# Optimization experiments

Hardware: AMD Instinct MI355X
Metric: run time of the kernel (lower is better)

Reference implementation:

```python
import jax, jax.numpy as jnp
import numpy as np

_EPS = 1e-6
B, N, W, R, NW = 64, 1024, 64, 4, 1


def _cosine_weights(memory, keys, strengths):
    # memory: [B,N,W], keys: [B,H,W], strengths: [B,H] -> [B,H,N]
    dot = jnp.einsum('bhw,bnw->bhn', keys, memory)
    mem_norm = jnp.sqrt(jnp.sum(memory * memory, axis=-1) + _EPS)  # [B,N]
    key_norm = jnp.sqrt(jnp.sum(keys * keys, axis=-1) + _EPS)      # [B,H]
    sim = dot / (key_norm[:, :, None] * mem_norm[:, None, :] + _EPS)
    sharp = sim * jax.nn.softplus(strengths)[:, :, None]
    return jax.nn.softmax(sharp, axis=-1)


def _allocation(usage):
    # usage: [B,N] -> allocation weights [B,N] (DNC sort-based free-list)
    usage = _EPS + (1.0 - _EPS) * usage
    nonusage = 1.0 - usage
    sorted_nonusage, indices = jax.lax.top_k(nonusage, N)
    sorted_usage = 1.0 - sorted_nonusage
    prod_excl = jnp.concatenate(
        [jnp.ones_like(sorted_usage[:, :1]), jnp.cumprod(sorted_usage[:, :-1], axis=-1)], axis=-1)
    sorted_alloc = sorted_nonusage * prod_excl
    inv_perm = jnp.argsort(indices, axis=-1)  # batch_invert_permutation
    return jnp.take_along_axis(sorted_alloc, inv_perm, axis=-1)  # batch_gather


def _forward(memory, prev_read_weights, prev_write_weights, prev_usage, prev_link,
             prev_precedence, read_keys, read_strengths, write_keys, write_strengths,
             write_vectors, erase_vectors, free_gate, alloc_gate, write_gate, read_mode):
    # ---- usage update (Freeness.call); prev write weights are stop-gradient'd ----
    ww = jax.lax.stop_gradient(prev_write_weights)
    agg_write = 1.0 - jnp.prod(1.0 - ww, axis=1)                       # [B,N]
    usage = prev_usage + (1.0 - prev_usage) * agg_write
    phi = jnp.prod(1.0 - free_gate[:, :, None] * prev_read_weights, axis=1)
    usage = usage * phi
    # ---- write weights: content + allocation ----
    write_content = _cosine_weights(memory, write_keys, write_strengths)  # [B,NW,N]
    wg = alloc_gate * write_gate                                          # [B,NW]
    allocs = []
    u = usage
    for i in range(NW):  # fixed small head loop
        a = _allocation(u)
        allocs.append(a)
        u = u + (1.0 - u) * wg[:, i:i + 1] * a
    alloc_w = jnp.stack(allocs, axis=1)                                   # [B,NW,N]
    ag = alloc_gate[:, :, None]
    write_weights = write_gate[:, :, None] * (ag * alloc_w + (1.0 - ag) * write_content)
    # ---- erase + write memory ----
    reset = jnp.prod(1.0 - write_weights[:, :, :, None] * erase_vectors[:, :, None, :], axis=1)
    memory_new = memory * reset + jnp.einsum('bwn,bwk->bnk', write_weights, write_vectors)
    # ---- temporal link matrix update ----
    wi = write_weights[:, :, :, None]   # [B,NW,N,1]
    wj = write_weights[:, :, None, :]   # [B,NW,1,N]
    new_link = (1.0 - wi - wj) * prev_link + wi * prev_precedence[:, :, None, :]
    link = new_link * (1.0 - jnp.eye(N, dtype=memory.dtype))[None, None]  # zero diagonal
    # (precedence update, part of new state; not needed for read_words output)
    precedence = (1.0 - jnp.sum(write_weights, axis=-1, keepdims=True)) * prev_precedence + write_weights
    del precedence
    # ---- read weights: content + directional (forward/backward along link) ----
    read_content = _cosine_weights(memory_new, read_keys, read_strengths)   # [B,R,N]
    fwd_w = jnp.einsum('brm,bwnm->brwn', prev_read_weights, link)           # adjoint_b=True
    bwd_w = jnp.einsum('brm,bwmn->brwn', prev_read_weights, link)
    mode = jax.nn.softmax(read_mode, axis=-1)                                # [B,R,2*NW+1]
    backward_mode = mode[:, :, :NW]
    forward_mode = mode[:, :, NW:2 * NW]
    content_mode = mode[:, :, 2 * NW]
    read_weights = (content_mode[:, :, None] * read_content
                    + jnp.einsum('brw,brwn->brn', forward_mode, fwd_w)
                    + jnp.einsum('brw,brwn->brn', backward_mode, bwd_w))
    read_words = jnp.einsum('brn,bnw->brw', read_weights, memory_new)        # [B,R,W]
    return read_words


def setup_inputs() -> dict:
    key = jax.random.key(0)
    ks = jax.random.split(key, 16)
    rn = lambda k, s: jax.random.normal(k, s, jnp.float32)
    ru = lambda k, s: jax.random.uniform(k, s, dtype=jnp.float32)
    return {
        'memory': rn(ks[0], (B, N, W)),
        'prev_read_weights': ru(ks[1], (B, R, N)),
        'prev_write_weights': ru(ks[2], (B, NW, N)),
        'prev_usage': ru(ks[3], (B, N)),
        'prev_link': ru(ks[4], (B, NW, N, N)),
        'prev_precedence': ru(ks[5], (B, NW, N)),
        'read_keys': rn(ks[6], (B, R, W)),
        'read_strengths': rn(ks[7], (B, R)),
        'write_keys': rn(ks[8], (B, NW, W)),
        'write_strengths': rn(ks[9], (B, NW)),
        'write_vectors': rn(ks[10], (B, NW, W)),
        'erase_vectors': ru(ks[11], (B, NW, W)),
        'free_gate': ru(ks[12], (B, R)),
        'alloc_gate': ru(ks[13], (B, NW)),
        'write_gate': ru(ks[14], (B, NW)),
        'read_mode': rn(ks[15], (B, R, 2 * NW + 1)),
    }


def reference(memory, prev_read_weights, prev_write_weights, prev_usage, prev_link,
              prev_precedence, read_keys, read_strengths, write_keys, write_strengths,
              write_vectors, erase_vectors, free_gate, alloc_gate, write_gate, read_mode):
    return _forward(memory, prev_read_weights, prev_write_weights, prev_usage, prev_link,
                    prev_precedence, read_keys, read_strengths, write_keys, write_strengths,
                    write_vectors, erase_vectors, free_gate, alloc_gate, write_gate, read_mode)
```

## Files before the change

kernel.cpp:

```cpp
#include <hip/hip_runtime.h>
#include <cmath>

#define NN 1024
#define BB 64
#define WD 64
#define RR 4

constexpr float EPSF = 1e-6f;

__device__ __forceinline__ float softplusf(float x) {
    return fmaxf(x, 0.f) + log1pf(expf(-fabsf(x)));
}

__device__ __forceinline__ float block_sum(float v, float* red, float* bc) {
#pragma unroll
    for (int o = 1; o < 64; o <<= 1) v += __shfl_xor(v, o, 64);
    const int wid = threadIdx.x >> 6, lane = threadIdx.x & 63;
    if (lane == 0) red[wid] = v;
    __syncthreads();
    if (wid == 0) {
        float x = (lane < 16) ? red[lane] : 0.f;
#pragma unroll
        for (int o = 1; o < 16; o <<= 1) x += __shfl_xor(x, o, 64);
        if (lane == 0) bc[0] = x;
    }
    __syncthreads();
    return bc[0];
}

__device__ __forceinline__ float block_max(float v, float* red, float* bc) {
#pragma unroll
    for (int o = 1; o < 64; o <<= 1) v = fmaxf(v, __shfl_xor(v, o, 64));
    const int wid = threadIdx.x >> 6, lane = threadIdx.x & 63;
    if (lane == 0) red[wid] = v;
    __syncthreads();
    if (wid == 0) {
        float x = (lane < 16) ? red[lane] : -INFINITY;
#pragma unroll
        for (int o = 1; o < 16; o <<= 1) x = fmaxf(x, __shfl_xor(x, o, 64));
        if (lane == 0) bc[0] = x;
    }
    __syncthreads();
    return bc[0];
}

__device__ __forceinline__ float4 block_sum4(float4 v, float4* red, float4* bc) {
#pragma unroll
    for (int o = 1; o < 64; o <<= 1) {
        v.x += __shfl_xor(v.x, o, 64); v.y += __shfl_xor(v.y, o, 64);
        v.z += __shfl_xor(v.z, o, 64); v.w += __shfl_xor(v.w, o, 64);
    }
    const int wid = threadIdx.x >> 6, lane = threadIdx.x & 63;
    if (lane == 0) red[wid] = v;
    __syncthreads();
    if (wid == 0) {
        float4 x;
        if (lane < 16) x = red[lane];
        else { x.x = 0.f; x.y = 0.f; x.z = 0.f; x.w = 0.f; }
#pragma unroll
        for (int o = 1; o < 16; o <<= 1) {
            x.x += __shfl_xor(x.x, o, 64); x.y += __shfl_xor(x.y, o, 64);
            x.z += __shfl_xor(x.z, o, 64); x.w += __shfl_xor(x.w, o, 64);
        }
        if (lane == 0) bc[0] = x;
    }
    __syncthreads();
    return bc[0];
}

__device__ __forceinline__ float4 block_max4(float4 v, float4* red, float4* bc) {
#pragma unroll
    for (int o = 1; o < 64; o <<= 1) {
        v.x = fmaxf(v.x, __shfl_xor(v.x, o, 64)); v.y = fmaxf(v.y, __shfl_xor(v.y, o, 64));
        v.z = fmaxf(v.z, __shfl_xor(v.z, o, 64)); v.w = fmaxf(v.w, __shfl_xor(v.w, o, 64));
    }
    const int wid = threadIdx.x >> 6, lane = threadIdx.x & 63;
    if (lane == 0) red[wid] = v;
    __syncthreads();
    if (wid == 0) {
        float4 x;
        if (lane < 16) x = red[lane];
        else { x.x = -INFINITY; x.y = -INFINITY; x.z = -INFINITY; x.w = -INFINITY; }
#pragma unroll
        for (int o = 1; o < 16; o <<= 1) {
            x.x = fmaxf(x.x, __shfl_xor(x.x, o, 64)); x.y = fmaxf(x.y, __shfl_xor(x.y, o, 64));
            x.z = fmaxf(x.z, __shfl_xor(x.z, o, 64)); x.w = fmaxf(x.w, __shfl_xor(x.w, o, 64));
        }
        if (lane == 0) bc[0] = x;
    }
    __syncthreads();
    return bc[0];
}

__global__ __launch_bounds__(1024) void prep_kernel(
    const float* __restrict__ memory, const float* __restrict__ prw,
    const float* __restrict__ pww, const float* __restrict__ pusage,
    const float* __restrict__ pprec,
    const float* __restrict__ rkeys_g, const float* __restrict__ rstr_g,
    const float* __restrict__ wkeys_g, const float* __restrict__ wstr_g,
    const float* __restrict__ wvec_g, const float* __restrict__ evec_g,
    const float* __restrict__ fg_g, const float* __restrict__ ag_g,
    const float* __restrict__ wg_g,
    float* __restrict__ wwG, float* __restrict__ rcG,
    float* __restrict__ SrpG, float* __restrict__ SuwwG,
    float* __restrict__ colU)
{
    __shared__ float wkey[WD], wvecS[WD], evecS[WD], rkey[RR * WD];
    __shared__ float skey[NN];
    __shared__ int   sidx[NN];
    __shared__ float pArr[NN], wcArr[NN], allocArr[NN];
    __shared__ float red1[16], bc1[1];
    __shared__ float4 red4[16], bc4[1];

    const int b = blockIdx.x, tid = threadIdx.x, n = tid;

#pragma unroll
    for (int k = 0; k < 8; ++k)
        colU[((size_t)b << 13) + (k << 10) + tid] = 0.f;

    if (tid < WD) {
        wkey[tid]  = wkeys_g[b * WD + tid];
        wvecS[tid] = wvec_g[b * WD + tid];
        evecS[tid] = evec_g[b * WD + tid];
    } else if (tid >= 128 && tid < 128 + RR * WD) {
        int k = tid - 128;
        rkey[k] = rkeys_g[b * RR * WD + k];
    }
    __syncthreads();

    float ur[RR];
#pragma unroll
    for (int r = 0; r < RR; ++r) ur[r] = prw[((size_t)b * RR + r) * NN + n];
    const float pw = pww[b * NN + n];
    const float pu = pusage[b * NN + n];
    float usage = pu + (1.f - pu) * pw;
    float phi = 1.f;
#pragma unroll
    for (int r = 0; r < RR; ++r) phi *= (1.f - fg_g[b * RR + r] * ur[r]);
    usage *= phi;

    const float* mrow = memory + ((size_t)b * NN + n) * WD;
    float dot = 0.f, nrm = 0.f, knrm = 0.f;
#pragma unroll 4
    for (int w4 = 0; w4 < WD / 4; ++w4) {
        const float4 m = *(const float4*)(mrow + w4 * 4);
        const float4 k = *(const float4*)(wkey + w4 * 4);
        dot  += m.x * k.x + m.y * k.y + m.z * k.z + m.w * k.w;
        nrm  += m.x * m.x + m.y * m.y + m.z * m.z + m.w * m.w;
        knrm += k.x * k.x + k.y * k.y + k.z * k.z + k.w * k.w;
    }
    const float sim = dot / (sqrtf(knrm + EPSF) * sqrtf(nrm + EPSF) + EPSF);
    const float sharp = sim * softplusf(wstr_g[b]);
    const float mxw = block_max(sharp, red1, bc1);
    const float exw = expf(sharp - mxw);
    const float smw = block_sum(exw, red1, bc1);
    wcArr[n] = exw / smw;

    const float ue = EPSF + (1.f - EPSF) * usage;
    skey[n] = 1.f - ue;
    sidx[n] = n;
    __syncthreads();
    for (int k = 2; k <= NN; k <<= 1) {
        for (int j = k >> 1; j > 0; j >>= 1) {
            const int ixj = tid ^ j;
            if (ixj > tid) {
                const float ka = skey[tid], kb = skey[ixj];
                const int ia = sidx[tid], ib = sidx[ixj];
                const bool precBA = (kb > ka) || (kb == ka && ib < ia);
                const bool precAB = (ka > kb) || (ka == kb && ia < ib);
                const bool dosw = ((tid & k) == 0) ? precBA : precAB;
                if (dosw) { skey[tid] = kb; skey[ixj] = ka; sidx[tid] = ib; sidx[ixj] = ia; }
            }
            __syncthreads();
        }
    }
    pArr[n] = (n == 0) ? 1.f : (1.f - skey[n - 1]);
    __syncthreads();
    for (int off = 1; off < NN; off <<= 1) {
        const float t = (n >= off) ? pArr[n - off] : 1.f;
        __syncthreads();
        pArr[n] *= t;
        __syncthreads();
    }
    allocArr[sidx[n]] = skey[n] * pArr[n];
    __syncthreads();

    const float agv = ag_g[b], wgv = wg_g[b];
    const float ww = wgv * (agv * allocArr[n] + (1.f - agv) * wcArr[n]);
    wwG[b * NN + n] = ww;

    float rdot0 = 0, rdot1 = 0, rdot2 = 0, rdot3 = 0, nn2 = 0;
    float rk0 = 0, rk1 = 0, rk2 = 0, rk3 = 0;
#pragma unroll 4
    for (int w4 = 0; w4 < WD / 4; ++w4) {
        const float4 m = *(const float4*)(mrow + w4 * 4);
        const float4 e = *(const float4*)(evecS + w4 * 4);
        const float4 v = *(const float4*)(wvecS + w4 * 4);
        float4 mn_;
        mn_.x = m.x * (1.f - ww * e.x) + ww * v.x;
        mn_.y = m.y * (1.f - ww * e.y) + ww * v.y;
        mn_.z = m.z * (1.f - ww * e.z) + ww * v.z;
        mn_.w = m.w * (1.f - ww * e.w) + ww * v.w;
        nn2 += mn_.x * mn_.x + mn_.y * mn_.y + mn_.z * mn_.z + mn_.w * mn_.w;
        const float4 k0 = *(const float4*)(rkey + 0 * WD + w4 * 4);
        const float4 k1 = *(const float4*)(rkey + 1 * WD + w4 * 4);
        const float4 k2 = *(const float4*)(rkey + 2 * WD + w4 * 4);
        const float4 k3 = *(const float4*)(rkey + 3 * WD + w4 * 4);
        rdot0 += k0.x * mn_.x + k0.y * mn_.y + k0.z * mn_.z + k0.w * mn_.w;
        rdot1 += k1.x * mn_.x + k1.y * mn_.y + k1.z * mn_.z + k1.w * mn_.w;
        rdot2 += k2.x * mn_.x + k2.y * mn_.y + k2.z * mn_.z + k2.w * mn_.w;
        rdot3 += k3.x * mn_.x + k3.y * mn_.y + k3.z * mn_.z + k3.w * mn_.w;
        rk0 += k0.x * k0.x + k0.y * k0.y + k0.z * k0.z + k0.w * k0.w;
        rk1 += k1.x * k1.x + k1.y * k1.y + k1.z * k1.z + k1.w * k1.w;
        rk2 += k2.x * k2.x + k2.y * k2.y + k2.z * k2.z + k2.w * k2.w;
        rk3 += k3.x * k3.x + k3.y * k3.y + k3.z * k3.z + k3.w * k3.w;
    }
    const float mnn = sqrtf(nn2 + EPSF);
    float4 sharp4;
    sharp4.x = rdot0 / (sqrtf(rk0 + EPSF) * mnn + EPSF) * softplusf(rstr_g[b * RR + 0]);
    sharp4.y = rdot1 / (sqrtf(rk1 + EPSF) * mnn + EPSF) * softplusf(rstr_g[b * RR + 1]);
    sharp4.z = rdot2 / (sqrtf(rk2 + EPSF) * mnn + EPSF) * softplusf(rstr_g[b * RR + 2]);
    sharp4.w = rdot3 / (sqrtf(rk3 + EPSF) * mnn + EPSF) * softplusf(rstr_g[b * RR + 3]);
    const float4 mx4 = block_max4(sharp4, red4, bc4);
    float4 e4;
    e4.x = expf(sharp4.x - mx4.x); e4.y = expf(sharp4.y - mx4.y);
    e4.z = expf(sharp4.z - mx4.z); e4.w = expf(sharp4.w - mx4.w);
    const float4 s4 = block_sum4(e4, red4, bc4);
    rcG[((size_t)b * RR + 0) * NN + n] = e4.x / s4.x;
    rcG[((size_t)b * RR + 1) * NN + n] = e4.y / s4.y;
    rcG[((size_t)b * RR + 2) * NN + n] = e4.z / s4.z;
    rcG[((size_t)b * RR + 3) * NN + n] = e4.w / s4.w;

    const float prec_n = pprec[b * NN + n];
    float4 sp4, sw4;
    sp4.x = ur[0] * prec_n; sp4.y = ur[1] * prec_n; sp4.z = ur[2] * prec_n; sp4.w = ur[3] * prec_n;
    const float4 SrpV = block_sum4(sp4, red4, bc4);
    sw4.x = ur[0] * ww; sw4.y = ur[1] * ww; sw4.z = ur[2] * ww; sw4.w = ur[3] * ww;
    const float4 SuwwV = block_sum4(sw4, red4, bc4);
    if (tid == 0) {
        SrpG[b * RR + 0] = SrpV.x; SrpG[b * RR + 1] = SrpV.y;
        SrpG[b * RR + 2] = SrpV.z; SrpG[b * RR + 3] = SrpV.w;
        SuwwG[b * RR + 0] = SuwwV.x; SuwwG[b * RR + 1] = SuwwV.y;
        SuwwG[b * RR + 2] = SuwwV.z; SuwwG[b * RR + 3] = SuwwV.w;
    }
}

__global__ __launch_bounds__(512, 4) void row_kernel(
    const float* __restrict__ L, const float* __restrict__ prw,
    const float* __restrict__ wwG,
    float* __restrict__ rowP,
    float* __restrict__ diagG)
{
    __shared__ float uS[4][NN];
    __shared__ float wS[NN];

    const int s = blockIdx.x, b = blockIdx.y;
    const int t = threadIdx.x, lane = t & 63, wid = t >> 6;

    for (int k = t; k < NN; k += 512) {
        wS[k] = wwG[(b << 10) + k];
#pragma unroll
        for (int r = 0; r < 4; ++r)
            uS[r][k] = prw[((size_t)(b * 4 + r) << 10) + k];
    }
    __syncthreads();

    const int n0 = (s << 4) + (wid << 1);
    const float* Lb = L + ((size_t)b << 20);
    const float* row0 = Lb + ((size_t)n0 << 10);
    const float* row1 = row0 + NN;

    float acc[2][8];
#pragma unroll
    for (int i = 0; i < 2; ++i)
#pragma unroll
        for (int v = 0; v < 8; ++v) acc[i][v] = 0.f;

#pragma unroll
    for (int c = 0; c < 4; ++c) {
        const int col = (c << 8) + (lane << 2);
        const float4 l0 = *(const float4*)&row0[col];
        const float4 l1 = *(const float4*)&row1[col];
        const float4 wv = *(const float4*)&wS[col];
        float4 w0, w1;
        w0.x = l0.x * wv.x; w0.y = l0.y * wv.y; w0.z = l0.z * wv.z; w0.w = l0.w * wv.w;
        w1.x = l1.x * wv.x; w1.y = l1.y * wv.y; w1.z = l1.z * wv.z; w1.w = l1.w * wv.w;
#pragma unroll
        for (int r = 0; r < 4; ++r) {
            const float4 uv = *(const float4*)&uS[r][col];
            acc[0][r]     = fmaf(l0.x, uv.x, fmaf(l0.y, uv.y, fmaf(l0.z, uv.z, fmaf(l0.w, uv.w, acc[0][r]))));
            acc[0][4 + r] = fmaf(w0.x, uv.x, fmaf(w0.y, uv.y, fmaf(w0.z, uv.z, fmaf(w0.w, uv.w, acc[0][4 + r]))));
            acc[1][r]     = fmaf(l1.x, uv.x, fmaf(l1.y, uv.y, fmaf(l1.z, uv.z, fmaf(l1.w, uv.w, acc[1][r]))));
            acc[1][4 + r] = fmaf(w1.x, uv.x, fmaf(w1.y, uv.y, fmaf(w1.z, uv.z, fmaf(w1.w, uv.w, acc[1][4 + r]))));
        }
    }

    if (lane < 2) {
        const int n = n0 + lane;
        diagG[(b << 10) + n] = Lb[((size_t)n << 10) + n];
    }

#pragma unroll
    for (int i = 0; i < 2; ++i)
#pragma unroll
        for (int v = 0; v < 8; ++v) {
            float x = acc[i][v];
            x += __shfl_xor(x, 1, 64);  x += __shfl_xor(x, 2, 64);
            x += __shfl_xor(x, 4, 64);  x += __shfl_xor(x, 8, 64);
            x += __shfl_xor(x, 16, 64); x += __shfl_xor(x, 32, 64);
            if (lane == i * 8 + v)
                rowP[(((size_t)b * 8 + v) << 10) + n0 + i] = x;
        }
}

__global__ __launch_bounds__(256, 4) void col_kernel(
    const float* __restrict__ L, const float* __restrict__ prw,
    const float* __restrict__ wwG,
    float* __restrict__ colU)
{
    __shared__ float sL[128][8];

    const int s = blockIdx.x, b = blockIdx.y;
    const int t = threadIdx.x;
    const int n0 = s << 7;

    if (t < 128) {
        const int n = n0 + t;
        const float ww = wwG[(b << 10) + n];
#pragma unroll
        for (int r = 0; r < 4; ++r) {
            const float u = prw[((size_t)(b * 4 + r) << 10) + n];
            sL[t][r]     = u;
            sL[t][4 + r] = u * ww;
        }
    }
    __syncthreads();

    const float* Lb = L + ((size_t)b << 20) + ((size_t)n0 << 10);
    const int col = t << 2;

    float4 cacc[8];
#pragma unroll
    for (int v = 0; v < 8; ++v) { cacc[v].x = 0.f; cacc[v].y = 0.f; cacc[v].z = 0.f; cacc[v].w = 0.f; }

#pragma unroll 4
    for (int i = 0; i < 128; ++i) {
        const float4 lv = *(const float4*)&Lb[((size_t)i << 10) + col];
        const float4 s0 = *(const float4*)&sL[i][0];
        const float4 s1 = *(const float4*)&sL[i][4];
        cacc[0].x = fmaf(lv.x, s0.x, cacc[0].x); cacc[0].y = fmaf(lv.y, s0.x, cacc[0].y);
        cacc[0].z = fmaf(lv.z, s0.x, cacc[0].z); cacc[0].w = fmaf(lv.w, s0.x, cacc[0].w);
        cacc[1].x = fmaf(lv.x, s0.y, cacc[1].x); cacc[1].y = fmaf(lv.y, s0.y, cacc[1].y);
        cacc[1].z = fmaf(lv.z, s0.y, cacc[1].z); cacc[1].w = fmaf(lv.w, s0.y, cacc[1].w);
        cacc[2].x = fmaf(lv.x, s0.z, cacc[2].x); cacc[2].y = fmaf(lv.y, s0.z, cacc[2].y);
        cacc[2].z = fmaf(lv.z, s0.z, cacc[2].z); cacc[2].w = fmaf(lv.w, s0.z, cacc[2].w);
        cacc[3].x = fmaf(lv.x, s0.w, cacc[3].x); cacc[3].y = fmaf(lv.y, s0.w, cacc[3].y);
        cacc[3].z = fmaf(lv.z, s0.w, cacc[3].z); cacc[3].w = fmaf(lv.w, s0.w, cacc[3].w);
        cacc[4].x = fmaf(lv.x, s1.x, cacc[4].x); cacc[4].y = fmaf(lv.y, s1.x, cacc[4].y);
        cacc[4].z = fmaf(lv.z, s1.x, cacc[4].z); cacc[4].w = fmaf(lv.w, s1.x, cacc[4].w);
        cacc[5].x = fmaf(lv.x, s1.y, cacc[5].x); cacc[5].y = fmaf(lv.y, s1.y, cacc[5].y);
        cacc[5].z = fmaf(lv.z, s1.y, cacc[5].z); cacc[5].w = fmaf(lv.w, s1.y, cacc[5].w);
        cacc[6].x = fmaf(lv.x, s1.z, cacc[6].x); cacc[6].y = fmaf(lv.y, s1.z, cacc[6].y);
        cacc[6].z = fmaf(lv.z, s1.z, cacc[6].z); cacc[6].w = fmaf(lv.w, s1.z, cacc[6].w);
        cacc[7].x = fmaf(lv.x, s1.w, cacc[7].x); cacc[7].y = fmaf(lv.y, s1.w, cacc[7].y);
        cacc[7].z = fmaf(lv.z, s1.w, cacc[7].z); cacc[7].w = fmaf(lv.w, s1.w, cacc[7].w);
    }

    const size_t base = ((size_t)b << 13) + col;
#pragma unroll
    for (int v = 0; v < 8; ++v) {
        unsafeAtomicAdd((float*)colU + base + (v << 10) + 0, cacc[v].x);
        unsafeAtomicAdd((float*)colU + base + (v << 10) + 1, cacc[v].y);
        unsafeAtomicAdd((float*)colU + base + (v << 10) + 2, cacc[v].z);
        unsafeAtomicAdd((float*)colU + base + (v << 10) + 3, cacc[v].w);
    }
}

__global__ __launch_bounds__(256) void combine_kernel(
    const float* __restrict__ memory, const float* __restrict__ prw,
    const float* __restrict__ pprec, const float* __restrict__ diagG,
    const float* __restrict__ evec_g, const float* __restrict__ wvec_g,
    const float* __restrict__ rmode_g,
    const float* __restrict__ wwG, const float* __restrict__ rcG,
    const float* __restrict__ rowP, const float* __restrict__ colU,
    const float* __restrict__ SrpG, const float* __restrict__ SuwwG,
    float* __restrict__ out)
{
    __shared__ float rwL[RR][256];
    __shared__ float wwS[256];

    const int b = blockIdx.y;
    const int n0 = blockIdx.x * 256;
    const int t = threadIdx.x;
    const int n = n0 + t;

    const float wwn = wwG[b * NN + n];
    wwS[t] = wwn;
    const float prec_n = pprec[b * NN + n];
    const float diag = diagG[(b << 10) + n];

#pragma unroll
    for (int r = 0; r < RR; ++r) {
        const size_t idx = ((size_t)b * RR + r) * NN + n;
        const float un = prw[idx];
        const float rc = rcG[idx];
        const float ru = rowP[(((size_t)b * 8 + r) << 10) + n];
        const float rv = rowP[(((size_t)b * 8 + 4 + r) << 10) + n];
        const float cuv = colU[((size_t)b << 13) + (r << 10) + n];
        const float cvv = colU[((size_t)b << 13) + ((4 + r) << 10) + n];
        const float Srp = SrpG[b * RR + r], Suww = SuwwG[b * RR + r];
        const float corr = un * (1.f - 2.f * wwn) * diag;
        const float fwd = (1.f - wwn) * ru - rv - corr + wwn * (Srp - un * prec_n);
        const float bwd = (1.f - wwn) * cuv - cvv - corr + prec_n * (Suww - un * wwn);
        const float m0 = rmode_g[((size_t)b * RR + r) * 3 + 0];
        const float m1 = rmode_g[((size_t)b * RR + r) * 3 + 1];
        const float m2 = rmode_g[((size_t)b * RR + r) * 3 + 2];
        const float mx = fmaxf(m0, fmaxf(m1, m2));
        const float e0 = expf(m0 - mx), e1 = expf(m1 - mx), e2 = expf(m2 - mx);
        const float inv = 1.f / (e0 + e1 + e2);
        rwL[r][t] = (e2 * inv) * rc + (e1 * inv) * fwd + (e0 * inv) * bwd;
    }
    __syncthreads();

    const int r = t >> 6, w = t & 63;
    const float ev = evec_g[b * WD + w], wv = wvec_g[b * WD + w];
    float acc = 0.f;
    const float* mb = memory + ((size_t)b * NN + n0) * WD;
#pragma unroll 8
    for (int i = 0; i < 256; ++i) {
        const float m = mb[(size_t)i * WD + w];
        const float wwi = wwS[i];
        const float mn_ = m * (1.f - wwi * ev) + wwi * wv;
        acc = fmaf(rwL[r][i], mn_, acc);
    }
    unsafeAtomicAdd(&out[((size_t)b * RR + r) * WD + w], acc);
}

extern "C" void kernel_launch(void* const* d_in, const int* in_sizes, int n_in,
                              void* d_out, int out_size, void* d_ws, size_t ws_size,
                              hipStream_t stream) {
    const float* memory = (const float*)d_in[0];
    const float* prw    = (const float*)d_in[1];
    const float* pww    = (const float*)d_in[2];
    const float* pusage = (const float*)d_in[3];
    const float* plink  = (const float*)d_in[4];
    const float* pprec  = (const float*)d_in[5];
    const float* rkeys  = (const float*)d_in[6];
    const float* rstr   = (const float*)d_in[7];
    const float* wkeys  = (const float*)d_in[8];
    const float* wstr   = (const float*)d_in[9];
    const float* wvec   = (const float*)d_in[10];
    const float* evec   = (const float*)d_in[11];
    const float* fg     = (const float*)d_in[12];
    const float* ag     = (const float*)d_in[13];
    const float* wg     = (const float*)d_in[14];
    const float* rmode  = (const float*)d_in[15];

    float* ws = (float*)d_ws;
    const size_t BN   = (size_t)BB * NN;
    const size_t BRN  = (size_t)BB * RR * NN;
    const size_t B8N  = (size_t)BB * 8 * NN;

    float* wwG   = ws;
    float* rcG   = wwG + BN;
    float* rowP  = rcG + BRN;
    float* colU  = rowP + B8N;
    float* diagG = colU + B8N;
    float* Srp   = diagG + BN;
    float* Suww  = Srp + (size_t)BB * RR;

    hipMemsetAsync(d_out, 0, (size_t)out_size * sizeof(float), stream);

    prep_kernel<<<BB, 1024, 0, stream>>>(memory, prw, pww, pusage, pprec,
                                         rkeys, rstr, wkeys, wstr, wvec, evec,
                                         fg, ag, wg, wwG, rcG, Srp, Suww, colU);
    row_kernel<<<dim3(64, BB), 512, 0, stream>>>(plink, prw, wwG, rowP, diagG);
    col_kernel<<<dim3(8, BB), 256, 0, stream>>>(plink, prw, wwG, colU);
    combine_kernel<<<dim3(4, BB), 256, 0, stream>>>(memory, prw, pprec, diagG,
                                                    evec, wvec, rmode,
                                                    wwG, rcG, rowP, colU,
                                                    Srp, Suww, (float*)d_out);
}
```

Measured before the change: 632.5 us.

## Fuse row and column link-matrix passes into one striped kernel

Merges the separate row-product and column-product kernels over the link matrix into a single kernel that streams each 64-row stripe once, computing column accumulations and per-row dot products (via wave shuffles) from the same loads. Column results are written as per-stripe partials instead of atomically added, and the combine kernel sums the 16 partials; the colU zeroing in prep is dropped. This aims to halve global reads of the large link tensor, at the cost of heavy per-row shuffle reductions, a larger partial buffer, and fewer, longer blocks.

```diff
diff --git a/kernel.cpp b/kernel.cpp
--- a/kernel.cpp
+++ b/kernel.cpp
@@ -5,6 +5,7 @@
 #define BB 64
 #define WD 64
 #define RR 4
+#define STRIPES 16
 
 constexpr float EPSF = 1e-6f;
 
@@ -102,8 +103,7 @@
     const float* __restrict__ fg_g, const float* __restrict__ ag_g,
     const float* __restrict__ wg_g,
     float* __restrict__ wwG, float* __restrict__ rcG,
-    float* __restrict__ SrpG, float* __restrict__ SuwwG,
-    float* __restrict__ colU)
+    float* __restrict__ SrpG, float* __restrict__ SuwwG)
 {
     __shared__ float wkey[WD], wvecS[WD], evecS[WD], rkey[RR * WD];
     __shared__ float skey[NN];
@@ -113,10 +113,6 @@
     __shared__ float4 red4[16], bc4[1];
 
     const int b = blockIdx.x, tid = threadIdx.x, n = tid;
-
-#pragma unroll
-    for (int k = 0; k < 8; ++k)
-        colU[((size_t)b << 13) + (k << 10) + tid] = 0.f;
 
     if (tid < WD) {
         wkey[tid]  = wkeys_g[b * WD + tid];
@@ -245,109 +241,61 @@
     }
 }
 
-__global__ __launch_bounds__(512, 4) void row_kernel(
+__global__ __launch_bounds__(256, 4) void link_fused_kernel(
     const float* __restrict__ L, const float* __restrict__ prw,
     const float* __restrict__ wwG,
     float* __restrict__ rowP,
+    float* __restrict__ colPart,
     float* __restrict__ diagG)
 {
-    __shared__ float uS[4][NN];
-    __shared__ float wS[NN];
+    __shared__ float sRow[64][8];
+    __shared__ float rowAcc[64][4][8];
 
     const int s = blockIdx.x, b = blockIdx.y;
     const int t = threadIdx.x, lane = t & 63, wid = t >> 6;
-
-    for (int k = t; k < NN; k += 512) {
-        wS[k] = wwG[(b << 10) + k];
-#pragma unroll
-        for (int r = 0; r < 4; ++r)
-            uS[r][k] = prw[((size_t)(b * 4 + r) << 10) + k];
-    }
-    __syncthreads();
-
-    const int n0 = (s << 4) + (wid << 1);
-    const float* Lb = L + ((size_t)b << 20);
-    const float* row0 = Lb + ((size_t)n0 << 10);
-    const float* row1 = row0 + NN;
-
-    float acc[2][8];
-#pragma unroll
-    for (int i = 0; i < 2; ++i)
-#pragma unroll
-        for (int v = 0; v < 8; ++v) acc[i][v] = 0.f;
-
-#pragma unroll
-    for (int c = 0; c < 4; ++c) {
-        const int col = (c << 8) + (lane << 2);
-        const float4 l0 = *(const float4*)&row0[col];
-        const float4 l1 = *(const float4*)&row1[col];
-        const float4 wv = *(const float4*)&wS[col];
-        float4 w0, w1;
-        w0.x = l0.x * wv.x; w0.y = l0.y * wv.y; w0.z = l0.z * wv.z; w0.w = l0.w * wv.w;
-        w1.x = l1.x * wv.x; w1.y = l1.y * wv.y; w1.z = l1.z * wv.z; w1.w = l1.w * wv.w;
-#pragma unroll
-        for (int r = 0; r < 4; ++r) {
-            const float4 uv = *(const float4*)&uS[r][col];
-            acc[0][r]     = fmaf(l0.x, uv.x, fmaf(l0.y, uv.y, fmaf(l0.z, uv.z, fmaf(l0.w, uv.w, acc[0][r]))));
-            acc[0][4 + r] = fmaf(w0.x, uv.x, fmaf(w0.y, uv.y, fmaf(w0.z, uv.z, fmaf(w0.w, uv.w, acc[0][4 + r]))));
-            acc[1][r]     = fmaf(l1.x, uv.x, fmaf(l1.y, uv.y, fmaf(l1.z, uv.z, fmaf(l1.w, uv.w, acc[1][r]))));
-            acc[1][4 + r] = fmaf(w1.x, uv.x, fmaf(w1.y, uv.y, fmaf(w1.z, uv.z, fmaf(w1.w, uv.w, acc[1][4 + r]))));
-        }
-    }
-
-    if (lane < 2) {
-        const int n = n0 + lane;
-        diagG[(b << 10) + n] = Lb[((size_t)n << 10) + n];
-    }
-
-#pragma unroll
-    for (int i = 0; i < 2; ++i)
-#pragma unroll
-        for (int v = 0; v < 8; ++v) {
-            float x = acc[i][v];
-            x += __shfl_xor(x, 1, 64);  x += __shfl_xor(x, 2, 64);
-            x += __shfl_xor(x, 4, 64);  x += __shfl_xor(x, 8, 64);
-            x += __shfl_xor(x, 16, 64); x += __shfl_xor(x, 32, 64);
-            if (lane == i * 8 + v)
-                rowP[(((size_t)b * 8 + v) << 10) + n0 + i] = x;
-        }
-}
-
-__global__ __launch_bounds__(256, 4) void col_kernel(
-    const float* __restrict__ L, const float* __restrict__ prw,
-    const float* __restrict__ wwG,
-    float* __restrict__ colU)
-{
-    __shared__ float sL[128][8];
-
-    const int s = blockIdx.x, b = blockIdx.y;
-    const int t = threadIdx.x;
-    const int n0 = s << 7;
-
-    if (t < 128) {
-        const int n = n0 + t;
-        const float ww = wwG[(b << 10) + n];
-#pragma unroll
-        for (int r = 0; r < 4; ++r) {
-            const float u = prw[((size_t)(b * 4 + r) << 10) + n];
-            sL[t][r]     = u;
-            sL[t][4 + r] = u * ww;
-        }
-    }
-    __syncthreads();
-
-    const float* Lb = L + ((size_t)b << 20) + ((size_t)n0 << 10);
+    const int i0 = s << 6;
     const int col = t << 2;
 
+    const float* ub = prw + ((size_t)(b * RR) << 10);
+    const float* wb = wwG + ((size_t)b << 10);
+    const float* Lb = L + ((size_t)b << 20) + ((size_t)i0 << 10);
+
+    if (t < 64) {
+        const int n = i0 + t;
+        const float ww = wb[n];
+#pragma unroll
+        for (int r = 0; r < RR; ++r) {
+            const float u = ub[(r << 10) + n];
+            sRow[t][r]     = u;
+            sRow[t][4 + r] = u * ww;
+        }
+        diagG[(b << 10) + n] = L[((size_t)b << 20) + ((size_t)n << 10) + n];
+    }
+
+    float4 ucu[4], ucw[4];
+    {
+        const float4 wwc = *(const float4*)&wb[col];
+#pragma unroll
+        for (int r = 0; r < RR; ++r) {
+            const float4 u = *(const float4*)&ub[(r << 10) + col];
+            ucu[r] = u;
+            ucw[r].x = u.x * wwc.x; ucw[r].y = u.y * wwc.y;
+            ucw[r].z = u.z * wwc.z; ucw[r].w = u.w * wwc.w;
+        }
+    }
+
     float4 cacc[8];
 #pragma unroll
     for (int v = 0; v < 8; ++v) { cacc[v].x = 0.f; cacc[v].y = 0.f; cacc[v].z = 0.f; cacc[v].w = 0.f; }
 
-#pragma unroll 4
-    for (int i = 0; i < 128; ++i) {
+    __syncthreads();
+
+#pragma unroll 2
+    for (int i = 0; i < 64; ++i) {
         const float4 lv = *(const float4*)&Lb[((size_t)i << 10) + col];
-        const float4 s0 = *(const float4*)&sL[i][0];
-        const float4 s1 = *(const float4*)&sL[i][4];
+
+        const float4 s0 = *(const float4*)&sRow[i][0];
+        const float4 s1 = *(const float4*)&sRow[i][4];
         cacc[0].x = fmaf(lv.x, s0.x, cacc[0].x); cacc[0].y = fmaf(lv.y, s0.x, cacc[0].y);
         cacc[0].z = fmaf(lv.z, s0.x, cacc[0].z); cacc[0].w = fmaf(lv.w, s0.x, cacc[0].w);
         cacc[1].x = fmaf(lv.x, s0.y, cacc[1].x); cacc[1].y = fmaf(lv.y, s0.y, cacc[1].y);
@@ -364,15 +312,40 @@
         cacc[6].z = fmaf(lv.z, s1.z, cacc[6].z); cacc[6].w = fmaf(lv.w, s1.z, cacc[6].w);
         cacc[7].x = fmaf(lv.x, s1.w, cacc[7].x); cacc[7].y = fmaf(lv.y, s1.w, cacc[7].y);
         cacc[7].z = fmaf(lv.z, s1.w, cacc[7].z); cacc[7].w = fmaf(lv.w, s1.w, cacc[7].w);
-    }
-
-    const size_t base = ((size_t)b << 13) + col;
-#pragma unroll
-    for (int v = 0; v < 8; ++v) {
-        unsafeAtomicAdd((float*)colU + base + (v << 10) + 0, cacc[v].x);
-        unsafeAtomicAdd((float*)colU + base + (v << 10) + 1, cacc[v].y);
-        unsafeAtomicAdd((float*)colU + base + (v << 10) + 2, cacc[v].z);
-        unsafeAtomicAdd((float*)colU + base + (v << 10) + 3, cacc[v].w);
+
+        float p[8];
+#pragma unroll
+        for (int r = 0; r < RR; ++r) {
+            p[r]     = fmaf(lv.x, ucu[r].x, fmaf(lv.y, ucu[r].y, fmaf(lv.z, ucu[r].z, lv.w * ucu[r].w)));
+            p[4 + r] = fmaf(lv.x, ucw[r].x, fmaf(lv.y, ucw[r].y, fmaf(lv.z, ucw[r].z, lv.w * ucw[r].w)));
+        }
+        float out = 0.f;
+#pragma unroll
+        for (int v = 0; v < 8; ++v) {
+            float x = p[v];
+            x += __shfl_xor(x, 1, 64);  x += __shfl_xor(x, 2, 64);
+            x += __shfl_xor(x, 4, 64);  x += __shfl_xor(x, 8, 64);
+            x += __shfl_xor(x, 16, 64); x += __shfl_xor(x, 32, 64);
+            if (lane == v) out = x;
+        }
+        if (lane < 8) rowAcc[i][wid][lane] = out;
+    }
+
+    {
+        const size_t base = (((size_t)s * BB + b) * 8) << 10;
+#pragma unroll
+        for (int v = 0; v < 8; ++v)
+            *(float4*)&colPart[base + ((size_t)v << 10) + col] = cacc[v];
+    }
+
+    __syncthreads();
+#pragma unroll
+    for (int k = 0; k < 2; ++k) {
+        const int idx = t + k * 256;
+        const int row = idx >> 3, v = idx & 7;
+        const float sum = rowAcc[row][0][v] + rowAcc[row][1][v]
+                        + rowAcc[row][2][v] + rowAcc[row][3][v];
+        rowP[(((size_t)b * 8 + v) << 10) + i0 + row] = sum;
     }
 }
 
@@ -382,7 +355,7 @@
     const float* __restrict__ evec_g, const float* __restrict__ wvec_g,
     const float* __restrict__ rmode_g,
     const float* __restrict__ wwG, const float* __restrict__ rcG,
-    const float* __restrict__ rowP, const float* __restrict__ colU,
+    const float* __restrict__ rowP, const float* __restrict__ colPart,
     const float* __restrict__ SrpG, const float* __restrict__ SuwwG,
     float* __restrict__ out)
 {
@@ -406,8 +379,13 @@
         const float rc = rcG[idx];
         const float ru = rowP[(((size_t)b * 8 + r) << 10) + n];
         const float rv = rowP[(((size_t)b * 8 + 4 + r) << 10) + n];
-        const float cuv = colU[((size_t)b << 13) + (r << 10) + n];
-        const float cvv = colU[((size_t)b << 13) + ((4 + r) << 10) + n];
+        float cuv = 0.f, cvv = 0.f;
+#pragma unroll
+        for (int s2 = 0; s2 < STRIPES; ++s2) {
+            const size_t base = (((size_t)s2 * BB + b) * 8) << 10;
+            cuv += colPart[base + ((size_t)r << 10) + n];
+            cvv += colPart[base + ((size_t)(4 + r) << 10) + n];
+        }
         const float Srp = SrpG[b * RR + r], Suww = SuwwG[b * RR + r];
         const float corr = un * (1.f - 2.f * wwn) * diag;
         const float fwd = (1.f - wwn) * ru - rv - corr + wwn * (Srp - un * prec_n);
@@ -460,12 +438,13 @@
     const size_t BN   = (size_t)BB * NN;
     const size_t BRN  = (size_t)BB * RR * NN;
     const size_t B8N  = (size_t)BB * 8 * NN;
+    const size_t COLP = (size_t)STRIPES * BB * 8 * NN;
 
     float* wwG   = ws;
     float* rcG   = wwG + BN;
     float* rowP  = rcG + BRN;
-    float* colU  = rowP + B8N;
-    float* diagG = colU + B8N;
+    float* colP  = rowP + B8N;
+    float* diagG = colP + COLP;
     float* Srp   = diagG + BN;
     float* Suww  = Srp + (size_t)BB * RR;
 
@@ -473,11 +452,11 @@
 
     prep_kernel<<<BB, 1024, 0, stream>>>(memory, prw, pww, pusage, pprec,
                                          rkeys, rstr, wkeys, wstr, wvec, evec,
-                                         fg, ag, wg, wwG, rcG, Srp, Suww, colU);
-    row_kernel<<<dim3(64, BB), 512, 0, stream>>>(plink, prw, wwG, rowP, diagG);
-    col_kernel<<<dim3(8, BB), 256, 0, stream>>>(plink, prw, wwG, colU);
+                                         fg, ag, wg, wwG, rcG, Srp, Suww);
+    link_fused_kernel<<<dim3(STRIPES, BB), 256, 0, stream>>>(plink, prw, wwG,
+                                                             rowP, colP, diagG);
     combine_kernel<<<dim3(4, BB), 256, 0, stream>>>(memory, prw, pprec, diagG,
                                                     evec, wvec, rmode,
-                                                    wwG, rcG, rowP, colU,
+                                                    wwG, rcG, rowP, colP,
                                                     Srp, Suww, (float*)d_out);
 }
```

Result: faster. 606.9 us (-4.0%).
